# Optimization experiments

Hardware: AMD Instinct MI355X
Metric: run time of the kernel (lower is better)

Reference implementation:

```python
import jax, jax.numpy as jnp
import numpy as np

DIM = 3072
HEADS = 24
HEAD_DIM = DIM // HEADS  # 128
B, L = 2, 2048


def setup_inputs() -> dict:
    key = jax.random.key(0)
    ks = jax.random.split(key, 6)
    x = jax.random.normal(ks[0], (B, L, DIM), dtype=jnp.float32)
    # Build a genuine rotary freqs_cis tensor: [1,1,L,D/2,2,2]
    half = HEAD_DIM // 2
    inv_freq = 1.0 / (10000.0 ** (jnp.arange(0, half, dtype=jnp.float32) / half))
    ang = jnp.arange(L, dtype=jnp.float32)[:, None] * inv_freq[None, :]  # [L, D/2]
    cos, sin = jnp.cos(ang), jnp.sin(ang)
    # rotation matrix [[cos, -sin],[sin, cos]] stacked on last two dims
    pe = jnp.stack(
        [jnp.stack([cos, -sin], axis=-1), jnp.stack([sin, cos], axis=-1)], axis=-2
    )  # [L, D/2, 2, 2]
    pe = pe[None, None]  # [1,1,L,D/2,2,2]
    Wqkv = jax.random.normal(ks[1], (3 * DIM, DIM), dtype=jnp.float32) * 0.02
    bqkv = jax.random.normal(ks[2], (3 * DIM,), dtype=jnp.float32) * 0.02
    q_scale = jnp.ones((HEAD_DIM,), dtype=jnp.float32)
    k_scale = jnp.ones((HEAD_DIM,), dtype=jnp.float32)
    Wproj = jax.random.normal(ks[3], (DIM, DIM), dtype=jnp.float32) * 0.02
    bproj = jax.random.normal(ks[4], (DIM,), dtype=jnp.float32) * 0.02
    return {"x": x, "pe": pe, "Wqkv": Wqkv, "bqkv": bqkv,
            "q_scale": q_scale, "k_scale": k_scale,
            "Wproj": Wproj, "bproj": bproj}


def _rms_norm(t, scale):
    # computed in fp32 like the torch module (eps=1e-6)
    rrms = jax.lax.rsqrt(jnp.mean(t * t, axis=-1, keepdims=True) + 1e-6)
    return t * rrms * scale


def _apply_rope(t, pe):
    # t: [B,H,L,D]; pe: [1,1,L,D/2,2,2]
    b, h, l, d = t.shape
    t2 = t.reshape(b, h, l, d // 2, 1, 2)
    out = pe[..., 0] * t2[..., 0] + pe[..., 1] * t2[..., 1]  # [B,H,L,D/2,2]
    return out.reshape(b, h, l, d)


def reference(x, pe, Wqkv, bqkv, q_scale, k_scale, Wproj, bproj):
    b, l, dim = x.shape
    d = q_scale.shape[0]
    h = dim // d
    qkv = x @ Wqkv.T + bqkv                       # [B,L,3*dim]
    qkv = qkv.reshape(b, l, 3, h, d)
    q, k, v = jnp.transpose(qkv, (2, 0, 3, 1, 4))  # each [B,H,L,D]
    q = _rms_norm(q, q_scale)
    k = _rms_norm(k, k_scale)
    q = _apply_rope(q, pe)
    k = _apply_rope(k, pe)
    scale = 1.0 / jnp.sqrt(jnp.float32(d))
    scores = jnp.einsum("bhqd,bhkd->bhqk", q, k) * scale
    attn = jax.nn.softmax(scores, axis=-1)
    out = jnp.einsum("bhqk,bhkd->bhqd", attn, v)  # [B,H,L,D]
    out = jnp.transpose(out, (0, 2, 1, 3)).reshape(b, l, h * d)
    return out @ Wproj.T + bproj
```

## Files before the change

### kernel.cpp

```cpp
#include <hip/hip_runtime.h>

#define DIM   3072
#define HEADS 24
#define HDIM  128
#define BB    2
#define LSEQ  2048
#define BL    4096
#define NQKV  9216

typedef __bf16 bf16;
typedef __bf16 bf16x8 __attribute__((ext_vector_type(8)));
typedef float  f32x4  __attribute__((ext_vector_type(4)));

__device__ __forceinline__ void async_cp16(void* lds, const void* gp) {
  __builtin_amdgcn_global_load_lds(
      (const __attribute__((address_space(1))) void*)gp,
      (__attribute__((address_space(3))) void*)lds, 16, 0, 0);
}

__global__ void sniff_dtype(const unsigned short* __restrict__ w, int* __restrict__ flag) {
  if (threadIdx.x == 0 && blockIdx.x == 0) {
    int big = 0;
    for (int i = 0; i < 64; ++i) {
      const int e = (w[i] >> 7) & 0xFF;
      if (e >= 127) ++big;
    }
    *flag = (big >= 4) ? 1 : 0;
  }
}

__global__ __launch_bounds__(256) void to_bf16(
    const void* __restrict__ src, bf16* __restrict__ dst, long n,
    const int* __restrict__ flag) {
  const bool f = (*flag != 0);
  long i = (long)blockIdx.x * blockDim.x + threadIdx.x;
  const long stride = (long)gridDim.x * blockDim.x;
  if (f) {
    const float* s = (const float*)src;
    for (; i < n; i += stride) dst[i] = (bf16)s[i];
  } else {
    const unsigned short* s = (const unsigned short*)src;
    unsigned short* d = (unsigned short*)dst;
    for (; i < n; i += stride) d[i] = s[i];
  }
}

__device__ __forceinline__ void stage_half(
    const bf16* __restrict__ g, int ldk, int row0, int k0,
    char* lds, int wave, int lane)
{
  #pragma unroll
  for (int j = 0; j < 2; ++j) {
    const int idx = (j*8 + wave)*64 + lane;
    const int r   = idx >> 3;
    const int sg  = idx & 7;
    const int gs  = sg ^ (r & 7);
    async_cp16(lds + idx*16,
               (const char*)(g + (size_t)(row0 + r)*ldk + k0) + gs*16);
  }
}

#define FRAG(base, row, ks) \
  (*(const bf16x8*)((base) + (size_t)(row)*128 + \
     (((((ks)*4) + quad) ^ ((row) & 7)) * 16)))

__global__ __launch_bounds__(512, 2) void gemm256(
    const bf16* __restrict__ A, const bf16* __restrict__ Bw,
    const bf16* __restrict__ bias, void* __restrict__ Cv,
    int M, int N, int K, const int* __restrict__ flag)
{
  extern __shared__ char sm[];
  const bool f32out = (flag != nullptr) && (*flag != 0);
  const int tid = threadIdx.x, wave = tid >> 6, lane = tid & 63;
  const int lm = lane & 15, quad = lane >> 4;
  const int wm = wave >> 2, wn = wave & 3;

  const int gx = gridDim.x, nwg = gx * gridDim.y;
  const int orig = blockIdx.y * gx + blockIdx.x;
  const int cpx = nwg >> 3;
  const int wg  = (orig & 7) * cpx + (orig >> 3);
  const int bm = (wg % gx) * 256;
  const int bn = (wg / gx) * 256;

  const int KT = K >> 6;

  f32x4 acc[8][4];
  const f32x4 zero4 = {0.f, 0.f, 0.f, 0.f};
  #pragma unroll
  for (int i = 0; i < 8; ++i)
    #pragma unroll
    for (int j = 0; j < 4; ++j) acc[i][j] = zero4;

  stage_half(A,  K, bm,       0, sm,          wave, lane);
  stage_half(A,  K, bm + 128, 0, sm + 16384,  wave, lane);
  stage_half(Bw, K, bn,       0, sm + 32768,  wave, lane);
  stage_half(Bw, K, bn + 128, 0, sm + 49152,  wave, lane);
  asm volatile("s_waitcnt vmcnt(0)" ::: "memory");
  __builtin_amdgcn_s_barrier();

  bf16x8 af[4][2], b0[2][2], b1[2][2];

  for (int kt = 0; kt < KT; ++kt) {
    const char* At = sm + (kt & 1) * 65536;
    const char* Bt = At + 32768;

    #pragma unroll
    for (int mf = 0; mf < 4; ++mf)
      #pragma unroll
      for (int ks = 0; ks < 2; ++ks)
        af[mf][ks] = FRAG(At, wm*128 + mf*16 + lm, ks);
    #pragma unroll
    for (int nf = 0; nf < 2; ++nf)
      #pragma unroll
      for (int ks = 0; ks < 2; ++ks)
        b0[nf][ks] = FRAG(Bt, wn*64 + nf*16 + lm, ks);
    if (kt + 1 < KT) {
      char* dA = sm + ((kt + 1) & 1) * 65536;
      const int k1 = (kt + 1) * 64;
      stage_half(A,  K, bm,       k1, dA,          wave, lane);
      stage_half(A,  K, bm + 128, k1, dA + 16384,  wave, lane);
      stage_half(Bw, K, bn,       k1, dA + 32768,  wave, lane);
      stage_half(Bw, K, bn + 128, k1, dA + 49152,  wave, lane);
    }
    __builtin_amdgcn_sched_barrier(0);
    __builtin_amdgcn_s_barrier();
    __builtin_amdgcn_s_setprio(1);
    #pragma unroll
    for (int mf = 0; mf < 4; ++mf)
      #pragma unroll
      for (int nf = 0; nf < 2; ++nf)
        #pragma unroll
        for (int ks = 0; ks < 2; ++ks)
          acc[mf][nf] = __builtin_amdgcn_mfma_f32_16x16x32_bf16(
              af[mf][ks], b0[nf][ks], acc[mf][nf], 0, 0, 0);
    __builtin_amdgcn_s_setprio(0);
    __builtin_amdgcn_sched_barrier(0);
    __builtin_amdgcn_s_barrier();

    #pragma unroll
    for (int nf = 0; nf < 2; ++nf)
      #pragma unroll
      for (int ks = 0; ks < 2; ++ks)
        b1[nf][ks] = FRAG(Bt, wn*64 + 32 + nf*16 + lm, ks);
    __builtin_amdgcn_sched_barrier(0);
    __builtin_amdgcn_s_barrier();
    __builtin_amdgcn_s_setprio(1);
    #pragma unroll
    for (int mf = 0; mf < 4; ++mf)
      #pragma unroll
      for (int nf = 0; nf < 2; ++nf)
        #pragma unroll
        for (int ks = 0; ks < 2; ++ks)
          acc[mf][2 + nf] = __builtin_amdgcn_mfma_f32_16x16x32_bf16(
              af[mf][ks], b1[nf][ks], acc[mf][2 + nf], 0, 0, 0);
    __builtin_amdgcn_s_setprio(0);
    __builtin_amdgcn_sched_barrier(0);
    __builtin_amdgcn_s_barrier();

    #pragma unroll
    for (int mf = 0; mf < 4; ++mf)
      #pragma unroll
      for (int ks = 0; ks < 2; ++ks)
        af[mf][ks] = FRAG(At, wm*128 + 64 + mf*16 + lm, ks);
    __builtin_amdgcn_sched_barrier(0);
    __builtin_amdgcn_s_barrier();
    __builtin_amdgcn_s_setprio(1);
    #pragma unroll
    for (int mf = 0; mf < 4; ++mf)
      #pragma unroll
      for (int nf = 0; nf < 2; ++nf)
        #pragma unroll
        for (int ks = 0; ks < 2; ++ks)
          acc[4 + mf][2 + nf] = __builtin_amdgcn_mfma_f32_16x16x32_bf16(
              af[mf][ks], b1[nf][ks], acc[4 + mf][2 + nf], 0, 0, 0);
    __builtin_amdgcn_s_setprio(0);
    __builtin_amdgcn_sched_barrier(0);
    __builtin_amdgcn_s_barrier();

    __builtin_amdgcn_s_setprio(1);
    #pragma unroll
    for (int mf = 0; mf < 4; ++mf)
      #pragma unroll
      for (int nf = 0; nf < 2; ++nf)
        #pragma unroll
        for (int ks = 0; ks < 2; ++ks)
          acc[4 + mf][nf] = __builtin_amdgcn_mfma_f32_16x16x32_bf16(
              af[mf][ks], b0[nf][ks], acc[4 + mf][nf], 0, 0, 0);
    __builtin_amdgcn_s_setprio(0);
    asm volatile("s_waitcnt vmcnt(0)" ::: "memory");
    __builtin_amdgcn_s_barrier();
  }

  #pragma unroll
  for (int ni = 0; ni < 4; ++ni) {
    const int col = bn + wn*64 + ni*16 + lm;
    const float bv = (float)bias[col];
    #pragma unroll
    for (int mi = 0; mi < 8; ++mi) {
      const int row0 = bm + wm*128 + mi*16 + quad*4;
      #pragma unroll
      for (int r = 0; r < 4; ++r) {
        const float v = acc[mi][ni][r] + bv;
        if (f32out) ((float*)Cv)[(size_t)(row0 + r)*N + col] = v;
        else        ((bf16*)Cv)[(size_t)(row0 + r)*N + col] = (bf16)v;
      }
    }
  }
}

__global__ __launch_bounds__(128) void norm_rope(
    bf16* __restrict__ qkv,
    const bf16* __restrict__ pe,
    const bf16* __restrict__ q_scale,
    const bf16* __restrict__ k_scale)
{
  const int blk = blockIdx.x;
  const int h  = blk % HEADS;
  const int bl = blk / HEADS;
  const int l  = bl & (LSEQ - 1);
  const int d  = threadIdx.x;

  bf16* row = qkv + (size_t)bl * NQKV;
  bf16* qp_ = row + h*HDIM + d;
  bf16* kp_ = row + DIM + h*HDIM + d;
  float qv = (float)*qp_;
  float kv = (float)*kp_;

  float sq = qv*qv, sk = kv*kv;
  #pragma unroll
  for (int off = 32; off >= 1; off >>= 1) {
    sq += __shfl_xor(sq, off);
    sk += __shfl_xor(sk, off);
  }
  __shared__ float red[4];
  const int wv = threadIdx.x >> 6;
  if ((threadIdx.x & 63) == 0) { red[wv*2] = sq; red[wv*2+1] = sk; }
  __syncthreads();
  const float rq = rsqrtf((red[0] + red[2]) * (1.f/HDIM) + 1e-6f);
  const float rk = rsqrtf((red[1] + red[3]) * (1.f/HDIM) + 1e-6f);

  qv = qv * rq * (float)q_scale[d];
  kv = kv * rk * (float)k_scale[d];

  const float qpn = __shfl_xor(qv, 1);
  const float kpn = __shfl_xor(kv, 1);
  const bf16* pp = pe + ((size_t)l*64 + (d >> 1))*4 + (d & 1)*2;
  const float c0 = (float)pp[0], c1 = (float)pp[1];
  const float qe = (d & 1) ? qpn : qv, qo = (d & 1) ? qv : qpn;
  const float ke = (d & 1) ? kpn : kv, ko = (d & 1) ? kv : kpn;
  float qr = c0*qe + c1*qo;
  float kr = c0*ke + c1*ko;
  qr *= 0.08838834764831845f;

  *qp_ = (bf16)qr;
  *kp_ = (bf16)kr;
}

__global__ __launch_bounds__(256) void v_transpose(
    const bf16* __restrict__ qkv, bf16* __restrict__ Vt)
{
  __shared__ bf16 tile[64][144];
  const int bid = blockIdx.x;
  const int lt = bid & 31;
  const int h  = (bid >> 5) % HEADS;
  const int b  = bid / (32*HEADS);
  const int l0 = lt * 64;
  const int tid = threadIdx.x;

  #pragma unroll
  for (int pass = 0; pass < 4; ++pass) {
    const int r = pass*16 + (tid >> 4);
    const int c = (tid & 15) * 8;
    const bf16* src = qkv + (size_t)(b*LSEQ + l0 + r)*NQKV + (2*DIM) + h*HDIM + c;
    *(uint4*)&tile[r][c] = *(const uint4*)src;
  }
  __syncthreads();
  #pragma unroll
  for (int pass = 0; pass < 4; ++pass) {
    const int d = pass*32 + (tid >> 3);
    const int c = (tid & 7) * 8;
    alignas(16) bf16 tmp[8];
    #pragma unroll
    for (int j = 0; j < 8; ++j) tmp[j] = tile[c + j][d];
    bf16* dst = Vt + (((size_t)b*HEADS + h)*HDIM + d)*LSEQ + l0 + c;
    *(uint4*)dst = *(const uint4*)tmp;
  }
}

__global__ __launch_bounds__(256, 2) void flash_attn(
    const bf16* __restrict__ qkv,
    const bf16* __restrict__ Vt,
    bf16* __restrict__ AO)
{
  extern __shared__ bf16 smem[];
  bf16* Ps = smem + 32768;

  const int bid = blockIdx.x;
  const int lt = bid & 15;
  const int h  = (bid >> 4) % HEADS;
  const int b  = bid / (16*HEADS);
  const int l0 = lt * 128;
  const int tid = threadIdx.x, wave = tid >> 6, lane = tid & 63;
  const int lm = lane & 15, quad = lane >> 4;

  const bf16* Qg = qkv + (size_t)(b*LSEQ)*NQKV + h*HDIM;
  const bf16* Kg = Qg + DIM;
  const bf16* Vg = Vt + (size_t)(b*HEADS + h)*HDIM*LSEQ;

  const int srow = lane >> 4;
  const int sg   = lane & 15;
  const int vrow = lane >> 3;
  const int vg   = lane & 7;

  #pragma unroll
  for (int j = 0; j < 8; ++j) {
    const int rl = wave*32 + j*4 + srow;
    const int g  = sg ^ (rl & 15);
    async_cp16((char*)smem + rl*256 + sg*16,
               (const char*)(Qg + (size_t)(l0 + rl)*NQKV + g*8));
  }
  __syncthreads();
  bf16x8 aq[2][4];
  #pragma unroll
  for (int half = 0; half < 2; ++half)
    #pragma unroll
    for (int ks = 0; ks < 4; ++ks)
      aq[half][ks] = *(const bf16x8*)
          &smem[(half*64 + wave*16 + lm)*128 + (((ks*4 + quad) ^ lm) * 8)];
  __syncthreads();

  const f32x4 zero4 = {0.f, 0.f, 0.f, 0.f};
  f32x4 o[2][8];
  float lp[2][4];
  #pragma unroll
  for (int s2 = 0; s2 < 2; ++s2) {
    #pragma unroll
    for (int dt = 0; dt < 8; ++dt) o[s2][dt] = zero4;
    #pragma unroll
    for (int r = 0; r < 4; ++r) lp[s2][r] = 0.f;
  }

  #pragma unroll
  for (int j = 0; j < 4; ++j) {
    const int rl = wave*16 + j*4 + srow;
    const int g  = sg ^ (rl & 15);
    async_cp16((char*)smem + rl*256 + sg*16,
               (const char*)(Kg + (size_t)rl*NQKV + g*8));
  }
  #pragma unroll
  for (int j = 0; j < 4; ++j) {
    const int dd = wave*32 + j*8 + vrow;
    const int g  = vg ^ (dd & 7);
    async_cp16((char*)smem + 32768 + dd*128 + vg*16,
               (const char*)(Vg + (size_t)dd*LSEQ + g*8));
  }

  for (int it = 0; it < LSEQ/64; ++it) {
    __syncthreads();
    const int cur = it & 1;
    if (it + 1 < LSEQ/64) {
      const int nxt = 1 - cur;
      const int kv0 = (it + 1) * 64;
      #pragma unroll
      for (int j = 0; j < 4; ++j) {
        const int rl = wave*16 + j*4 + srow;
        const int g  = sg ^ (rl & 15);
        async_cp16((char*)smem + nxt*16384 + rl*256 + sg*16,
                   (const char*)(Kg + (size_t)(kv0 + rl)*NQKV + g*8));
      }
      #pragma unroll
      for (int j = 0; j < 4; ++j) {
        const int dd = wave*32 + j*8 + vrow;
        const int g  = vg ^ (dd & 7);
        async_cp16((char*)smem + 32768 + nxt*16384 + dd*128 + vg*16,
                   (const char*)(Vg + (size_t)dd*LSEQ + kv0 + g*8));
      }
    }

    const bf16* Ksb = smem + cur*8192;
    const bf16* Vsb = smem + 16384 + cur*8192;

    f32x4 s[2][4];
    #pragma unroll
    for (int s2 = 0; s2 < 2; ++s2)
      #pragma unroll
      for (int nt = 0; nt < 4; ++nt) s[s2][nt] = zero4;
    #pragma unroll
    for (int nt = 0; nt < 4; ++nt) {
      bf16x8 bk[4];
      #pragma unroll
      for (int ks = 0; ks < 4; ++ks)
        bk[ks] = *(const bf16x8*)
            &Ksb[(nt*16 + lm)*128 + (((ks*4 + quad) ^ lm) * 8)];
      #pragma unroll
      for (int half = 0; half < 2; ++half)
        #pragma unroll
        for (int ks = 0; ks < 4; ++ks)
          s[half][nt] = __builtin_amdgcn_mfma_f32_16x16x32_bf16(
              aq[half][ks], bk[ks], s[half][nt], 0, 0, 0);
    }

    #pragma unroll
    for (int half = 0; half < 2; ++half)
      #pragma unroll
      for (int r = 0; r < 4; ++r) {
        const int pr = quad*4 + r;
        #pragma unroll
        for (int nt = 0; nt < 4; ++nt) {
          const float e = __expf(s[half][nt][r]);
          const bf16 pb = (bf16)e;
          Ps[wave*2048 + half*1024 + pr*64 +
             (((nt*2 + (lm >> 3)) ^ (pr & 7)) * 8) + (lm & 7)] = pb;
          lp[half][r] += (float)pb;
        }
      }

    #pragma unroll
    for (int ks2 = 0; ks2 < 2; ++ks2) {
      const int psl = (((ks2*4 + quad) ^ (lm & 7)) * 8);
      const bf16x8 ap0 = *(const bf16x8*)&Ps[wave*2048 +        lm*64 + psl];
      const bf16x8 ap1 = *(const bf16x8*)&Ps[wave*2048 + 1024 + lm*64 + psl];
      #pragma unroll
      for (int dt = 0; dt < 8; ++dt) {
        bf16x8 bv = *(const bf16x8*)&Vsb[(dt*16 + lm)*64 + psl];
        o[0][dt] = __builtin_amdgcn_mfma_f32_16x16x32_bf16(ap0, bv, o[0][dt], 0, 0, 0);
        o[1][dt] = __builtin_amdgcn_mfma_f32_16x16x32_bf16(ap1, bv, o[1][dt], 0, 0, 0);
      }
    }
  }

  #pragma unroll
  for (int half = 0; half < 2; ++half)
    #pragma unroll
    for (int r = 0; r < 4; ++r) {
      float v = lp[half][r];
      v += __shfl_xor(v, 1);
      v += __shfl_xor(v, 2);
      v += __shfl_xor(v, 4);
      v += __shfl_xor(v, 8);
      const float rli = 1.f / v;
      const int row = b*LSEQ + l0 + half*64 + wave*16 + quad*4 + r;
      #pragma unroll
      for (int dt = 0; dt < 8; ++dt) {
        const int col = h*HDIM + dt*16 + lm;
        AO[(size_t)row*DIM + col] = (bf16)(o[half][dt][r] * rli);
      }
    }
}

extern "C" void kernel_launch(void* const* d_in, const int* in_sizes, int n_in,
                              void* d_out, int out_size, void* d_ws, size_t ws_size,
                              hipStream_t stream)
{
  (void)in_sizes; (void)n_in; (void)out_size; (void)ws_size;
  bf16* ws = (bf16*)d_ws;
  int*  flag = (int*)d_ws;
  bf16* cx  = ws + 128;
  bf16* cWq = cx  + (size_t)BL*DIM;
  bf16* cWp = cWq + (size_t)NQKV*DIM;
  bf16* cpe = cWp + (size_t)DIM*DIM;
  bf16* cbq = cpe + (size_t)LSEQ*256;
  bf16* cbp = cbq + NQKV;
  bf16* cqs = cbp + DIM;
  bf16* cks = cqs + HDIM;
  bf16* qkv = cks + HDIM;
  bf16* Vt  = cWq;
  bf16* AO  = cx;

  static bool attr_set = false;
  if (!attr_set) {
    hipFuncSetAttribute((const void*)flash_attn,
                        hipFuncAttributeMaxDynamicSharedMemorySize, 81920);
    hipFuncSetAttribute((const void*)gemm256,
                        hipFuncAttributeMaxDynamicSharedMemorySize, 131072);
    attr_set = true;
  }

  hipLaunchKernelGGL(sniff_dtype, dim3(1), dim3(64), 0, stream,
                     (const unsigned short*)d_in[2], flag);
  hipLaunchKernelGGL(to_bf16, dim3(4096), dim3(256), 0, stream,
                     d_in[0], cx,  (long)BL*DIM, flag);
  hipLaunchKernelGGL(to_bf16, dim3(4096), dim3(256), 0, stream,
                     d_in[2], cWq, (long)NQKV*DIM, flag);
  hipLaunchKernelGGL(to_bf16, dim3(4096), dim3(256), 0, stream,
                     d_in[6], cWp, (long)DIM*DIM, flag);
  hipLaunchKernelGGL(to_bf16, dim3(512), dim3(256), 0, stream,
                     d_in[1], cpe, (long)LSEQ*256, flag);
  hipLaunchKernelGGL(to_bf16, dim3(36), dim3(256), 0, stream,
                     d_in[3], cbq, (long)NQKV, flag);
  hipLaunchKernelGGL(to_bf16, dim3(12), dim3(256), 0, stream,
                     d_in[7], cbp, (long)DIM, flag);
  hipLaunchKernelGGL(to_bf16, dim3(1), dim3(256), 0, stream,
                     d_in[4], cqs, (long)HDIM, flag);
  hipLaunchKernelGGL(to_bf16, dim3(1), dim3(256), 0, stream,
                     d_in[5], cks, (long)HDIM, flag);

  hipLaunchKernelGGL(gemm256, dim3(BL/256, NQKV/256), dim3(512), 131072, stream,
                     cx, cWq, cbq, qkv, BL, NQKV, DIM, (const int*)nullptr);
  hipLaunchKernelGGL(norm_rope, dim3(BL*HEADS), dim3(128), 0, stream,
                     qkv, cpe, cqs, cks);
  hipLaunchKernelGGL(v_transpose, dim3(BB*HEADS*(LSEQ/64)), dim3(256), 0, stream,
                     qkv, Vt);
  hipLaunchKernelGGL(flash_attn, dim3(BB*HEADS*(LSEQ/128)), dim3(256), 81920, stream,
                     qkv, Vt, AO);
  hipLaunchKernelGGL(gemm256, dim3(BL/256, DIM/256), dim3(512), 131072, stream,
                     AO, cWp, cbp, d_out, BL, DIM, DIM, flag);
}
```

Measured before the change: 804.4 us.

## Switch GEMM to 4-stage K=32 LDS pipeline with partial vmcnt waits

Replaces the double-buffered K=64 GEMM main loop with a four-buffer ring of K=32 tiles, prefetching three tiles ahead and waiting only on the oldest loads through partial vmcnt counts. The goal is to hide global-to-LDS latency behind MFMA work, which the old loop's full vmcnt(0) wait each iteration did not do. The XOR swizzle is dropped in favour of plain 64-byte rows, so LDS fragment reads may now hit bank conflicts. Each tile also carries half as much MFMA work per barrier, so barrier overhead per unit of compute goes up.

```diff
diff --git a/kernel.cpp b/kernel.cpp
--- a/kernel.cpp
+++ b/kernel.cpp
@@ -45,24 +45,74 @@
   }
 }
 
-__device__ __forceinline__ void stage_half(
+__device__ __forceinline__ void stage_one(
     const bf16* __restrict__ g, int ldk, int row0, int k0,
-    char* lds, int wave, int lane)
-{
-  #pragma unroll
-  for (int j = 0; j < 2; ++j) {
-    const int idx = (j*8 + wave)*64 + lane;
-    const int r   = idx >> 3;
-    const int sg  = idx & 7;
-    const int gs  = sg ^ (r & 7);
-    async_cp16(lds + idx*16,
-               (const char*)(g + (size_t)(row0 + r)*ldk + k0) + gs*16);
-  }
-}
-
-#define FRAG(base, row, ks) \
-  (*(const bf16x8*)((base) + (size_t)(row)*128 + \
-     (((((ks)*4) + quad) ^ ((row) & 7)) * 16)))
+    char* ldsbase, int idx)
+{
+  const int r = idx >> 2, sl = idx & 3;
+  async_cp16(ldsbase + idx*16,
+             (const char*)(g + (size_t)(row0 + r)*ldk + k0 + sl*8));
+}
+
+template<int WAITN, bool STAGE>
+__device__ __forceinline__ void ktile(
+    const bf16* __restrict__ A, const bf16* __restrict__ Bw,
+    char* __restrict__ sm, int kt, int K, int bm, int bn,
+    int tid, int wm, int wn, int lm, int quad, f32x4 (&acc)[8][4])
+{
+  const char* At = sm + (size_t)(kt & 3) * 32768;
+  const char* Bt = At + 16384;
+  char* buf3 = sm + (size_t)((kt + 3) & 3) * 32768;
+  const int k3 = (kt + 3) * 32;
+
+  bf16x8 af[4], bfr[4];
+
+  #pragma unroll
+  for (int mf = 0; mf < 4; ++mf)
+    af[mf] = *(const bf16x8*)(At + (size_t)(wm*128 + mf*16 + lm)*64 + quad*16);
+  #pragma unroll
+  for (int nf = 0; nf < 4; ++nf)
+    bfr[nf] = *(const bf16x8*)(Bt + (size_t)(wn*64 + nf*16 + lm)*64 + quad*16);
+  if (STAGE) {
+    stage_one(A, K, bm, k3, buf3, tid);
+    stage_one(A, K, bm, k3, buf3, 512 + tid);
+  }
+  __builtin_amdgcn_sched_barrier(0);
+  __builtin_amdgcn_s_barrier();
+  __builtin_amdgcn_s_setprio(1);
+  #pragma unroll
+  for (int mf = 0; mf < 4; ++mf)
+    #pragma unroll
+    for (int nf = 0; nf < 4; ++nf)
+      acc[mf][nf] = __builtin_amdgcn_mfma_f32_16x16x32_bf16(
+          af[mf], bfr[nf], acc[mf][nf], 0, 0, 0);
+  __builtin_amdgcn_s_setprio(0);
+  __builtin_amdgcn_sched_barrier(0);
+  __builtin_amdgcn_s_barrier();
+
+  #pragma unroll
+  for (int mf = 0; mf < 4; ++mf)
+    af[mf] = *(const bf16x8*)(At + (size_t)(wm*128 + 64 + mf*16 + lm)*64 + quad*16);
+  if (STAGE) {
+    stage_one(Bw, K, bn, k3, buf3 + 16384, tid);
+    stage_one(Bw, K, bn, k3, buf3 + 16384, 512 + tid);
+  }
+  __builtin_amdgcn_sched_barrier(0);
+  __builtin_amdgcn_s_barrier();
+  __builtin_amdgcn_s_setprio(1);
+  #pragma unroll
+  for (int mf = 0; mf < 4; ++mf)
+    #pragma unroll
+    for (int nf = 0; nf < 4; ++nf)
+      acc[4 + mf][nf] = __builtin_amdgcn_mfma_f32_16x16x32_bf16(
+          af[mf], bfr[nf], acc[4 + mf][nf], 0, 0, 0);
+  __builtin_amdgcn_s_setprio(0);
+  if (WAITN == 8)      asm volatile("s_waitcnt vmcnt(8)" ::: "memory");
+  else if (WAITN == 4) asm volatile("s_waitcnt vmcnt(4)" ::: "memory");
+  else if (WAITN == 0) asm volatile("s_waitcnt vmcnt(0)" ::: "memory");
+  __builtin_amdgcn_sched_barrier(0);
+  __builtin_amdgcn_s_barrier();
+}
 
 __global__ __launch_bounds__(512, 2) void gemm256(
     const bf16* __restrict__ A, const bf16* __restrict__ Bw,
@@ -82,7 +132,7 @@
   const int bm = (wg % gx) * 256;
   const int bn = (wg / gx) * 256;
 
-  const int KT = K >> 6;
+  const int KT = K >> 5;
 
   f32x4 acc[8][4];
   const f32x4 zero4 = {0.f, 0.f, 0.f, 0.f};
@@ -91,105 +141,24 @@
     #pragma unroll
     for (int j = 0; j < 4; ++j) acc[i][j] = zero4;
 
-  stage_half(A,  K, bm,       0, sm,          wave, lane);
-  stage_half(A,  K, bm + 128, 0, sm + 16384,  wave, lane);
-  stage_half(Bw, K, bn,       0, sm + 32768,  wave, lane);
-  stage_half(Bw, K, bn + 128, 0, sm + 49152,  wave, lane);
-  asm volatile("s_waitcnt vmcnt(0)" ::: "memory");
+  #pragma unroll
+  for (int t = 0; t < 3; ++t) {
+    char* bt = sm + (size_t)t * 32768;
+    const int k0 = t * 32;
+    stage_one(A,  K, bm, k0, bt,         tid);
+    stage_one(A,  K, bm, k0, bt,         512 + tid);
+    stage_one(Bw, K, bn, k0, bt + 16384, tid);
+    stage_one(Bw, K, bn, k0, bt + 16384, 512 + tid);
+  }
+  asm volatile("s_waitcnt vmcnt(8)" ::: "memory");
   __builtin_amdgcn_s_barrier();
 
-  bf16x8 af[4][2], b0[2][2], b1[2][2];
-
-  for (int kt = 0; kt < KT; ++kt) {
-    const char* At = sm + (kt & 1) * 65536;
-    const char* Bt = At + 32768;
-
-    #pragma unroll
-    for (int mf = 0; mf < 4; ++mf)
-      #pragma unroll
-      for (int ks = 0; ks < 2; ++ks)
-        af[mf][ks] = FRAG(At, wm*128 + mf*16 + lm, ks);
-    #pragma unroll
-    for (int nf = 0; nf < 2; ++nf)
-      #pragma unroll
-      for (int ks = 0; ks < 2; ++ks)
-        b0[nf][ks] = FRAG(Bt, wn*64 + nf*16 + lm, ks);
-    if (kt + 1 < KT) {
-      char* dA = sm + ((kt + 1) & 1) * 65536;
-      const int k1 = (kt + 1) * 64;
-      stage_half(A,  K, bm,       k1, dA,          wave, lane);
-      stage_half(A,  K, bm + 128, k1, dA + 16384,  wave, lane);
-      stage_half(Bw, K, bn,       k1, dA + 32768,  wave, lane);
-      stage_half(Bw, K, bn + 128, k1, dA + 49152,  wave, lane);
-    }
-    __builtin_amdgcn_sched_barrier(0);
-    __builtin_amdgcn_s_barrier();
-    __builtin_amdgcn_s_setprio(1);
-    #pragma unroll
-    for (int mf = 0; mf < 4; ++mf)
-      #pragma unroll
-      for (int nf = 0; nf < 2; ++nf)
-        #pragma unroll
-        for (int ks = 0; ks < 2; ++ks)
-          acc[mf][nf] = __builtin_amdgcn_mfma_f32_16x16x32_bf16(
-              af[mf][ks], b0[nf][ks], acc[mf][nf], 0, 0, 0);
-    __builtin_amdgcn_s_setprio(0);
-    __builtin_amdgcn_sched_barrier(0);
-    __builtin_amdgcn_s_barrier();
-
-    #pragma unroll
-    for (int nf = 0; nf < 2; ++nf)
-      #pragma unroll
-      for (int ks = 0; ks < 2; ++ks)
-        b1[nf][ks] = FRAG(Bt, wn*64 + 32 + nf*16 + lm, ks);
-    __builtin_amdgcn_sched_barrier(0);
-    __builtin_amdgcn_s_barrier();
-    __builtin_amdgcn_s_setprio(1);
-    #pragma unroll
-    for (int mf = 0; mf < 4; ++mf)
-      #pragma unroll
-      for (int nf = 0; nf < 2; ++nf)
-        #pragma unroll
-        for (int ks = 0; ks < 2; ++ks)
-          acc[mf][2 + nf] = __builtin_amdgcn_mfma_f32_16x16x32_bf16(
-              af[mf][ks], b1[nf][ks], acc[mf][2 + nf], 0, 0, 0);
-    __builtin_amdgcn_s_setprio(0);
-    __builtin_amdgcn_sched_barrier(0);
-    __builtin_amdgcn_s_barrier();
-
-    #pragma unroll
-    for (int mf = 0; mf < 4; ++mf)
-      #pragma unroll
-      for (int ks = 0; ks < 2; ++ks)
-        af[mf][ks] = FRAG(At, wm*128 + 64 + mf*16 + lm, ks);
-    __builtin_amdgcn_sched_barrier(0);
-    __builtin_amdgcn_s_barrier();
-    __builtin_amdgcn_s_setprio(1);
-    #pragma unroll
-    for (int mf = 0; mf < 4; ++mf)
-      #pragma unroll
-      for (int nf = 0; nf < 2; ++nf)
-        #pragma unroll
-        for (int ks = 0; ks < 2; ++ks)
-          acc[4 + mf][2 + nf] = __builtin_amdgcn_mfma_f32_16x16x32_bf16(
-              af[mf][ks], b1[nf][ks], acc[4 + mf][2 + nf], 0, 0, 0);
-    __builtin_amdgcn_s_setprio(0);
-    __builtin_amdgcn_sched_barrier(0);
-    __builtin_amdgcn_s_barrier();
-
-    __builtin_amdgcn_s_setprio(1);
-    #pragma unroll
-    for (int mf = 0; mf < 4; ++mf)
-      #pragma unroll
-      for (int nf = 0; nf < 2; ++nf)
-        #pragma unroll
-        for (int ks = 0; ks < 2; ++ks)
-          acc[4 + mf][nf] = __builtin_amdgcn_mfma_f32_16x16x32_bf16(
-              af[mf][ks], b0[nf][ks], acc[4 + mf][nf], 0, 0, 0);
-    __builtin_amdgcn_s_setprio(0);
-    asm volatile("s_waitcnt vmcnt(0)" ::: "memory");
-    __builtin_amdgcn_s_barrier();
-  }
+  int kt = 0;
+  for (; kt < KT - 3; ++kt)
+    ktile<8, true >(A, Bw, sm, kt, K, bm, bn, tid, wm, wn, lm, quad, acc);
+  ktile<4, false>(A, Bw, sm, kt, K, bm, bn, tid, wm, wn, lm, quad, acc); ++kt;
+  ktile<0, false>(A, Bw, sm, kt, K, bm, bn, tid, wm, wn, lm, quad, acc); ++kt;
+  ktile<-1, false>(A, Bw, sm, kt, K, bm, bn, tid, wm, wn, lm, quad, acc);
 
   #pragma unroll
   for (int ni = 0; ni < 4; ++ni) {
```

Result: no change. 813.2 us (+1.1%).
